# Kernel optimization log

Hardware: AMD Instinct MI355X
Metric: run time of the kernel (lower is better)

## Reference

```python
import jax, jax.numpy as jnp
import numpy as np

N, T, D, H = 64, 512, 1024, 1024

def setup_inputs() -> dict:
    key = jax.random.key(0)
    k1, k2, k3, k4 = jax.random.split(key, 4)
    x = jax.random.normal(k1, (N, T, D), dtype=jnp.float32)
    h0 = jax.random.normal(k2, (N, H), dtype=jnp.float32)
    Wx = jax.random.normal(k3, (D, 4 * H), dtype=jnp.float32) / np.sqrt(D)
    Wh = jax.random.normal(k4, (H, 4 * H), dtype=jnp.float32) / np.sqrt(H)
    b = jnp.zeros((4 * H,), dtype=jnp.float32)
    return {"x": x, "h0": h0, "Wx": Wx, "Wh": Wh, "b": b}

def reference(x, h0, Wx, Wh, b):
    # Hoist the input projection out of the recurrence: (N,T,D)@(D,4H) -> (N,T,4H)
    Hdim = h0.shape[1]
    xW = jnp.einsum('ntd,dg->ntg', x, Wx) + b  # (N, T, 4H)
    c0 = jnp.zeros_like(h0)

    def step(carry, xw_t):
        prev_h, prev_c = carry
        A = xw_t + prev_h @ Wh  # (N, 4H)
        i = jax.nn.sigmoid(A[:, 0:Hdim])
        f = jax.nn.sigmoid(A[:, Hdim:2 * Hdim])
        o = jax.nn.sigmoid(A[:, 2 * Hdim:3 * Hdim])
        g = jnp.tanh(A[:, 3 * Hdim:4 * Hdim])
        next_c = f * prev_c + i * g
        next_h = o * jnp.tanh(next_c)
        return (next_h, next_c), next_h

    # scan over time: xW transposed to (T, N, 4H)
    _, hs = jax.lax.scan(step, (h0, c0), jnp.swapaxes(xW, 0, 1))
    return jnp.swapaxes(hs, 0, 1)  # (N, T, H)
```

## Files before the change

### kernel.cpp

```cpp
#include <hip/hip_runtime.h>
#include <hip/hip_bf16.h>


#define T_T 512
#define KTOT 2048

typedef short bf16x8 __attribute__((ext_vector_type(8)));
typedef float f32x4 __attribute__((ext_vector_type(4)));
typedef unsigned u32x4 __attribute__((ext_vector_type(4)));

union B8U { u32x4 u; bf16x8 v; };
union P4 { __hip_bfloat16 h[4]; uint2 u; };

__device__ __forceinline__ float fsig(float x) {
  float e = __builtin_amdgcn_exp2f(-1.442695041f * x);
  return __builtin_amdgcn_rcpf(1.f + e);
}
__device__ __forceinline__ float ftanh(float x) {
  float e = __builtin_amdgcn_exp2f(2.885390082f * fabsf(x));
  float r = 1.f - 2.f * __builtin_amdgcn_rcpf(e + 1.f);
  return copysignf(r, x);
}

__global__ __launch_bounds__(256) void prep_weights(const float* __restrict__ Wx,
                                                    const float* __restrict__ Wh,
                                                    __hip_bfloat16* __restrict__ Wt) {
  __shared__ float tile[64][65];
  int kb = blockIdx.x & 31;
  int cb = blockIdx.x >> 5;
  int k0 = kb << 6, c0 = cb << 6;
  const float* W = (k0 < 1024) ? Wx : Wh;
  int kr0 = k0 & 1023;
  int tid = threadIdx.x;
  int f4 = tid & 15;
  int i0 = tid >> 4;
  for (int p = 0; p < 4; ++p) {
    int i = i0 + (p << 4);
    float4 v = *(const float4*)(W + (size_t)(kr0 + i) * 4096 + c0 + (f4 << 2));
    tile[(f4 << 2) + 0][i] = v.x;
    tile[(f4 << 2) + 1][i] = v.y;
    tile[(f4 << 2) + 2][i] = v.z;
    tile[(f4 << 2) + 3][i] = v.w;
  }
  __syncthreads();
  for (int p = 0; p < 16; ++p) {
    int idx = (p << 8) + tid;
    int kl = idx & 63, cl = idx >> 6;
    Wt[(size_t)(c0 + cl) * KTOT + k0 + kl] = __float2bfloat16(tile[cl][kl]);
  }
}

__global__ __launch_bounds__(256) void prep_xb(const float* __restrict__ x,
                                               __hip_bfloat16* __restrict__ xb) {
  int b = blockIdx.x;
  int n = b & 63, t = b >> 6;
  const float4* src = (const float4*)(x + ((size_t)n * T_T + t) * 1024);
  __hip_bfloat16* dst = xb + ((size_t)t * 64 + n) * 1024;
  float4 v = src[threadIdx.x];
  P4 pk;
  pk.h[0] = __float2bfloat16(v.x);
  pk.h[1] = __float2bfloat16(v.y);
  pk.h[2] = __float2bfloat16(v.z);
  pk.h[3] = __float2bfloat16(v.w);
  *(uint2*)(dst + (threadIdx.x << 2)) = pk.u;
}

__global__ __launch_bounds__(256) void prep_state(const float* __restrict__ h0,
                                                  __hip_bfloat16* __restrict__ hb) {
  int i = blockIdx.x * 256 + threadIdx.x;
  hb[i] = __float2bfloat16(h0[i]);
}

__global__ __launch_bounds__(512, 2) void lstm_persist(
    const __hip_bfloat16* __restrict__ xb,
    const float* __restrict__ bias,
    const __hip_bfloat16* __restrict__ Wt,
    __hip_bfloat16* hb,
    float* __restrict__ out,
    unsigned* flags)
{
  __shared__ __align__(16) __hip_bfloat16 AX[2][16][1032];
  __shared__ __align__(16) __hip_bfloat16 AH[16][1032];
  __shared__ float gtX[4][16][17];
  __shared__ float gtH[4][16][17];
  __shared__ __align__(16) __hip_bfloat16 hrow[16][16];
  __shared__ unsigned xcnt;

  const int tid  = threadIdx.x;
  const int cgrp = blockIdx.x & 63;
  const int bg   = blockIdx.x >> 6;
  const int rows0 = bg << 4;
  const int lane = tid & 63;
  const int wv   = tid >> 6;
  const int gate = wv & 3;
  const int half = wv >> 2;
  const int mcol = lane & 15;
  const int q    = lane >> 4;
  const int tid2 = tid & 255;

  if (tid == 0) xcnt = 0;

  u32x4 wfrag[32];
  {
    const __hip_bfloat16* wp = Wt
      + ((size_t)(gate << 10) + (cgrp << 4) + mcol) * (size_t)KTOT
      + (half << 10) + (q << 3);
    #pragma unroll
    for (int kk = 0; kk < 32; ++kk)
      wfrag[kk] = *(const u32x4*)(wp + (kk << 5));
  }

  const int er = tid2 >> 4, ej = tid2 & 15;
  const int hcol = (cgrp << 4) + ej;
  const int rg = rows0 + er;
  float b_i = 0.f, b_f = 0.f, b_o = 0.f, b_g = 0.f;
  if (half == 0) {
    b_i = bias[hcol]; b_f = bias[1024 + hcol];
    b_o = bias[2048 + hcol]; b_g = bias[3072 + hcol];
  }
  float creg = 0.f;
  int poison = 0;

  if (half == 0) {
    const u32x4* src = (const u32x4*)(xb + (size_t)rows0 * 1024);
    #pragma unroll
    for (int p = 0; p < 8; ++p) {
      int r = (p << 1) + (tid2 >> 7), c8 = tid2 & 127;
      u32x4 v = src[r * 128 + c8];
      *(u32x4*)&AX[0][r][c8 << 3] = v;
    }
  } else {
    const u32x4* src = (const u32x4*)(hb + (size_t)rows0 * 1024);
    #pragma unroll
    for (int p = 0; p < 8; ++p) {
      int r = (p << 1) + (tid2 >> 7), c8 = tid2 & 127;
      u32x4 v = src[r * 128 + c8];
      *(u32x4*)&AH[r][c8 << 3] = v;
    }
  }
  __syncthreads();

  for (int t = 0; t < T_T; ++t) {
    {
      const __hip_bfloat16* L = (half == 0) ? &AX[t & 1][0][0] : &AH[0][0];
      f32x4 acc = {0.f, 0.f, 0.f, 0.f};
      #pragma unroll
      for (int kk = 0; kk < 32; ++kk) {
        B8U a, b;
        a.u = *(const u32x4*)(L + (size_t)mcol * 1032 + (kk << 5) + (q << 3));
        b.u = wfrag[kk];
        acc = __builtin_amdgcn_mfma_f32_16x16x32_bf16(a.v, b.v, acc, 0, 0, 0);
      }
      float (*gt)[16][17] = (half == 0) ? gtX : gtH;
      #pragma unroll
      for (int i = 0; i < 4; ++i)
        gt[gate][(q << 2) + i][mcol] = acc[i];
    }
    __syncthreads();
    if (half == 0) {
      float av_i = gtX[0][er][ej] + gtH[0][er][ej] + b_i;
      float av_f = gtX[1][er][ej] + gtH[1][er][ej] + b_f;
      float av_o = gtX[2][er][ej] + gtH[2][er][ej] + b_o;
      float av_g = gtX[3][er][ej] + gtH[3][er][ej] + b_g;
      float iv = fsig(av_i), fv = fsig(av_f), ov = fsig(av_o);
      float gv = ftanh(av_g);
      float cn = fv * creg + iv * gv;
      creg = cn;
      float hv = ov * ftanh(cn);
      out[((size_t)rg * T_T + t) * 1024 + hcol] = hv;
      hrow[er][ej] = __float2bfloat16(hv);
      if (lane == 0)
        __hip_atomic_fetch_add(&xcnt, 1u, __ATOMIC_RELAXED, __HIP_MEMORY_SCOPE_WORKGROUP);
      if (wv == 0) {
        int spun = 0;
        while (!poison) {
          unsigned v = __hip_atomic_load(&xcnt, __ATOMIC_RELAXED,
                                         __HIP_MEMORY_SCOPE_WORKGROUP);
          if (v == 4u) break;
          if (++spun > (1 << 20)) poison = 1;
        }
        if (lane < 32) {
          u32x4 v = *(const u32x4*)&hrow[lane >> 1][(lane & 1) << 3];
          __hip_bfloat16* hd = hb + ((size_t)((t + 1) & 1) << 16)
                             + (size_t)(rows0 + (lane >> 1)) * 1024
                             + (cgrp << 4) + ((lane & 1) << 3);
          asm volatile("global_store_dwordx4 %0, %1, off sc0 sc1"
                       :: "v"(hd), "v"(v) : "memory");
        }
        asm volatile("s_waitcnt vmcnt(0)" ::: "memory");
        if (lane == 0) {
          __hip_atomic_store(&xcnt, 0u, __ATOMIC_RELAXED, __HIP_MEMORY_SCOPE_WORKGROUP);
          __hip_atomic_store(flags + ((unsigned)t << 8) + ((unsigned)bg << 6) + cgrp, 1u,
                             __ATOMIC_RELAXED, __HIP_MEMORY_SCOPE_AGENT);
        }
      }
      if (t + 1 < T_T) {
        const u32x4* src = (const u32x4*)(xb + ((size_t)(t + 1) * 64 + rows0) * 1024);
        #pragma unroll
        for (int p = 0; p < 8; ++p) {
          int r = (p << 1) + (tid2 >> 7), c8 = tid2 & 127;
          u32x4 v = src[r * 128 + c8];
          *(u32x4*)&AX[(t + 1) & 1][r][c8 << 3] = v;
        }
      }
    } else if (t + 1 < T_T) {
      const int chunk = wv - 4;
      {
        unsigned* fp = flags + ((unsigned)t << 8) + ((unsigned)bg << 6)
                     + (chunk << 4) + (lane & 15);
        int spun = 0;
        while (!poison) {
          unsigned v = __hip_atomic_load(fp, __ATOMIC_RELAXED, __HIP_MEMORY_SCOPE_AGENT);
          if (__all(v != 0)) break;
          __builtin_amdgcn_s_sleep(1);
          if (++spun > (1 << 16)) poison = 1;
        }
      }
      {
        const __hip_bfloat16* hsrc = hb + ((size_t)((t + 1) & 1) << 16);
        const int c8 = lane & 31;
        const int r0 = lane >> 5;
        const char* base = (const char*)(hsrc + (size_t)(rows0 + r0) * 1024
                                         + (chunk << 8) + (c8 << 3));
        const char* p0 = base;          const char* p1 = base + 4096;
        const char* p2 = base + 8192;   const char* p3 = base + 12288;
        const char* p4 = base + 16384;  const char* p5 = base + 20480;
        const char* p6 = base + 24576;  const char* p7 = base + 28672;
        u32x4 d0, d1, d2, d3, d4, d5, d6, d7;
        asm volatile(
          "global_load_dwordx4 %0, %8, off sc0 sc1\n\t"
          "global_load_dwordx4 %1, %9, off sc0 sc1\n\t"
          "global_load_dwordx4 %2, %10, off sc0 sc1\n\t"
          "global_load_dwordx4 %3, %11, off sc0 sc1\n\t"
          "global_load_dwordx4 %4, %12, off sc0 sc1\n\t"
          "global_load_dwordx4 %5, %13, off sc0 sc1\n\t"
          "global_load_dwordx4 %6, %14, off sc0 sc1\n\t"
          "global_load_dwordx4 %7, %15, off sc0 sc1\n\t"
          "s_waitcnt vmcnt(0)"
          : "=&v"(d0), "=&v"(d1), "=&v"(d2), "=&v"(d3),
            "=&v"(d4), "=&v"(d5), "=&v"(d6), "=&v"(d7)
          : "v"(p0), "v"(p1), "v"(p2), "v"(p3),
            "v"(p4), "v"(p5), "v"(p6), "v"(p7)
          : "memory");
        const int cc = (chunk << 8) + (c8 << 3);
        *(u32x4*)&AH[r0 +  0][cc] = d0;
        *(u32x4*)&AH[r0 +  2][cc] = d1;
        *(u32x4*)&AH[r0 +  4][cc] = d2;
        *(u32x4*)&AH[r0 +  6][cc] = d3;
        *(u32x4*)&AH[r0 +  8][cc] = d4;
        *(u32x4*)&AH[r0 + 10][cc] = d5;
        *(u32x4*)&AH[r0 + 12][cc] = d6;
        *(u32x4*)&AH[r0 + 14][cc] = d7;
      }
    }
    __syncthreads();
  }
}

extern "C" void kernel_launch(void* const* d_in, const int* in_sizes, int n_in,
                              void* d_out, int out_size, void* d_ws, size_t ws_size,
                              hipStream_t stream) {
  const float* x    = (const float*)d_in[0];
  const float* h0   = (const float*)d_in[1];
  const float* Wx   = (const float*)d_in[2];
  const float* Wh   = (const float*)d_in[3];
  const float* bias = (const float*)d_in[4];
  float* out = (float*)d_out;

  char* ws = (char*)d_ws;
  __hip_bfloat16* Wt  = (__hip_bfloat16*)ws;
  __hip_bfloat16* xb  = (__hip_bfloat16*)(ws + ((size_t)16 << 20));
  __hip_bfloat16* hbf = (__hip_bfloat16*)(ws + ((size_t)80 << 20));
  unsigned* flags     = (unsigned*)(ws + ((size_t)80 << 20) + (1u << 18));

  hipLaunchKernelGGL(prep_weights, dim3(2048), dim3(256), 0, stream, Wx, Wh, Wt);
  hipLaunchKernelGGL(prep_xb, dim3(32768), dim3(256), 0, stream, x, xb);
  hipLaunchKernelGGL(prep_state, dim3(256), dim3(256), 0, stream, h0, hbf);
  (void)hipMemsetAsync(flags, 0, (size_t)512 * 4 * 64 * sizeof(unsigned), stream);

  void* kargs[6];
  kargs[0] = (void*)&xb;
  kargs[1] = (void*)&bias;
  kargs[2] = (void*)&Wt;
  kargs[3] = (void*)&hbf;
  kargs[4] = (void*)&out;
  kargs[5] = (void*)&flags;
  (void)hipLaunchCooperativeKernel(lstm_persist, dim3(256), dim3(512), kargs, 0, stream);
}
```

Baseline: 3.792 ms.

## Move x-projection off the critical path and split recurrent matmul across all waves

The x-projection MFMA for step t+1 now runs on the first half of the waves after they publish h_t, using weights streamed from global memory, with double-buffered gate results. The recurrent h@Wh matmul is split in K across all eight waves, halving the serial per-step chain. The change also adds an XOR swizzle to the LDS layout, moves the output store after the flag publication, and removes the sleep from the flag spin. The cost is extra global weight traffic for Wx each step and a shorter spin timeout that could poison earlier.

```diff
diff --git a/kernel.cpp b/kernel.cpp
--- a/kernel.cpp
+++ b/kernel.cpp
@@ -20,6 +20,10 @@
   float e = __builtin_amdgcn_exp2f(2.885390082f * fabsf(x));
   float r = 1.f - 2.f * __builtin_amdgcn_rcpf(e + 1.f);
   return copysignf(r, x);
+}
+
+__device__ __forceinline__ int swz(int r, int cb) {
+  return (r << 11) + (cb ^ ((r & 7) << 4));
 }
 
 __global__ __launch_bounds__(256) void prep_weights(const float* __restrict__ Wx,
@@ -79,10 +83,10 @@
     float* __restrict__ out,
     unsigned* flags)
 {
-  __shared__ __align__(16) __hip_bfloat16 AX[2][16][1032];
-  __shared__ __align__(16) __hip_bfloat16 AH[16][1032];
-  __shared__ float gtX[4][16][17];
-  __shared__ float gtH[4][16][17];
+  __shared__ __align__(16) unsigned char AX[2][32768];
+  __shared__ __align__(16) unsigned char AH[32768];
+  __shared__ float gtH[2][4][16][20];
+  __shared__ float gtX[2][4][16][20];
   __shared__ __align__(16) __hip_bfloat16 hrow[16][16];
   __shared__ unsigned xcnt;
 
@@ -93,6 +97,7 @@
   const int lane = tid & 63;
   const int wv   = tid >> 6;
   const int gate = wv & 3;
+  const int kh   = wv >> 2;
   const int half = wv >> 2;
   const int mcol = lane & 15;
   const int q    = lane >> 4;
@@ -100,15 +105,17 @@
 
   if (tid == 0) xcnt = 0;
 
-  u32x4 wfrag[32];
+  u32x4 wfragH[16];
   {
     const __hip_bfloat16* wp = Wt
       + ((size_t)(gate << 10) + (cgrp << 4) + mcol) * (size_t)KTOT
-      + (half << 10) + (q << 3);
-    #pragma unroll
-    for (int kk = 0; kk < 32; ++kk)
-      wfrag[kk] = *(const u32x4*)(wp + (kk << 5));
-  }
+      + 1024 + (kh << 9) + (q << 3);
+    #pragma unroll
+    for (int kk = 0; kk < 16; ++kk)
+      wfragH[kk] = *(const u32x4*)(wp + (kk << 5));
+  }
+  const __hip_bfloat16* wpx = Wt
+    + ((size_t)(wv << 10) + (cgrp << 4) + mcol) * (size_t)KTOT + (q << 3);
 
   const int er = tid2 >> 4, ej = tid2 & 15;
   const int hcol = (cgrp << 4) + ej;
@@ -127,7 +134,7 @@
     for (int p = 0; p < 8; ++p) {
       int r = (p << 1) + (tid2 >> 7), c8 = tid2 & 127;
       u32x4 v = src[r * 128 + c8];
-      *(u32x4*)&AX[0][r][c8 << 3] = v;
+      *(u32x4*)(&AX[0][0] + swz(r, c8 << 4)) = v;
     }
   } else {
     const u32x4* src = (const u32x4*)(hb + (size_t)rows0 * 1024);
@@ -135,43 +142,64 @@
     for (int p = 0; p < 8; ++p) {
       int r = (p << 1) + (tid2 >> 7), c8 = tid2 & 127;
       u32x4 v = src[r * 128 + c8];
-      *(u32x4*)&AH[r][c8 << 3] = v;
+      *(u32x4*)(&AH[0] + swz(r, c8 << 4)) = v;
+    }
+  }
+  __syncthreads();
+  if (half == 0) {
+    f32x4 a0 = {0,0,0,0}, a1 = {0,0,0,0};
+    #pragma unroll 8
+    for (int kk = 0; kk < 32; ++kk) {
+      B8U a, b;
+      a.u = *(const u32x4*)(&AX[0][0] + swz(mcol, (kk << 6) + (q << 4)));
+      b.u = *(const u32x4*)(wpx + (kk << 5));
+      if (kk & 1) a1 = __builtin_amdgcn_mfma_f32_16x16x32_bf16(a.v, b.v, a1, 0, 0, 0);
+      else        a0 = __builtin_amdgcn_mfma_f32_16x16x32_bf16(a.v, b.v, a0, 0, 0, 0);
+    }
+    #pragma unroll
+    for (int i = 0; i < 4; ++i)
+      gtX[0][gate][(q << 2) + i][mcol] = a0[i] + a1[i];
+    const u32x4* src = (const u32x4*)(xb + ((size_t)64 + rows0) * 1024);
+    #pragma unroll
+    for (int p = 0; p < 8; ++p) {
+      int r = (p << 1) + (tid2 >> 7), c8 = tid2 & 127;
+      u32x4 v = src[r * 128 + c8];
+      *(u32x4*)(&AX[1][0] + swz(r, c8 << 4)) = v;
     }
   }
   __syncthreads();
 
   for (int t = 0; t < T_T; ++t) {
     {
-      const __hip_bfloat16* L = (half == 0) ? &AX[t & 1][0][0] : &AH[0][0];
-      f32x4 acc = {0.f, 0.f, 0.f, 0.f};
+      f32x4 a0 = {0,0,0,0}, a1 = {0,0,0,0};
+      const int kbase = kh << 10;
       #pragma unroll
-      for (int kk = 0; kk < 32; ++kk) {
+      for (int kk = 0; kk < 16; ++kk) {
         B8U a, b;
-        a.u = *(const u32x4*)(L + (size_t)mcol * 1032 + (kk << 5) + (q << 3));
-        b.u = wfrag[kk];
-        acc = __builtin_amdgcn_mfma_f32_16x16x32_bf16(a.v, b.v, acc, 0, 0, 0);
-      }
-      float (*gt)[16][17] = (half == 0) ? gtX : gtH;
+        a.u = *(const u32x4*)(&AH[0] + swz(mcol, kbase + (kk << 6) + (q << 4)));
+        b.u = wfragH[kk];
+        if (kk & 1) a1 = __builtin_amdgcn_mfma_f32_16x16x32_bf16(a.v, b.v, a1, 0, 0, 0);
+        else        a0 = __builtin_amdgcn_mfma_f32_16x16x32_bf16(a.v, b.v, a0, 0, 0, 0);
+      }
       #pragma unroll
       for (int i = 0; i < 4; ++i)
-        gt[gate][(q << 2) + i][mcol] = acc[i];
+        gtH[kh][gate][(q << 2) + i][mcol] = a0[i] + a1[i];
     }
     __syncthreads();
     if (half == 0) {
-      float av_i = gtX[0][er][ej] + gtH[0][er][ej] + b_i;
-      float av_f = gtX[1][er][ej] + gtH[1][er][ej] + b_f;
-      float av_o = gtX[2][er][ej] + gtH[2][er][ej] + b_o;
-      float av_g = gtX[3][er][ej] + gtH[3][er][ej] + b_g;
+      float av_i = gtX[t & 1][0][er][ej] + gtH[0][0][er][ej] + gtH[1][0][er][ej] + b_i;
+      float av_f = gtX[t & 1][1][er][ej] + gtH[0][1][er][ej] + gtH[1][1][er][ej] + b_f;
+      float av_o = gtX[t & 1][2][er][ej] + gtH[0][2][er][ej] + gtH[1][2][er][ej] + b_o;
+      float av_g = gtX[t & 1][3][er][ej] + gtH[0][3][er][ej] + gtH[1][3][er][ej] + b_g;
       float iv = fsig(av_i), fv = fsig(av_f), ov = fsig(av_o);
       float gv = ftanh(av_g);
       float cn = fv * creg + iv * gv;
       creg = cn;
       float hv = ov * ftanh(cn);
-      out[((size_t)rg * T_T + t) * 1024 + hcol] = hv;
       hrow[er][ej] = __float2bfloat16(hv);
       if (lane == 0)
         __hip_atomic_fetch_add(&xcnt, 1u, __ATOMIC_RELAXED, __HIP_MEMORY_SCOPE_WORKGROUP);
-      if (wv == 0) {
+      if (wv == 0 && t + 1 < T_T) {
         int spun = 0;
         while (!poison) {
           unsigned v = __hip_atomic_load(&xcnt, __ATOMIC_RELAXED,
@@ -193,14 +221,33 @@
           __hip_atomic_store(flags + ((unsigned)t << 8) + ((unsigned)bg << 6) + cgrp, 1u,
                              __ATOMIC_RELAXED, __HIP_MEMORY_SCOPE_AGENT);
         }
-      }
+      } else if (wv == 0 && lane == 0) {
+        __hip_atomic_store(&xcnt, 0u, __ATOMIC_RELAXED, __HIP_MEMORY_SCOPE_WORKGROUP);
+      }
+      out[((size_t)rg * T_T + t) * 1024 + hcol] = hv;
       if (t + 1 < T_T) {
-        const u32x4* src = (const u32x4*)(xb + ((size_t)(t + 1) * 64 + rows0) * 1024);
+        const unsigned char* L = &AX[(t + 1) & 1][0];
+        f32x4 a0 = {0,0,0,0}, a1 = {0,0,0,0};
+        #pragma unroll 8
+        for (int kk = 0; kk < 32; ++kk) {
+          B8U a, b;
+          a.u = *(const u32x4*)(L + swz(mcol, (kk << 6) + (q << 4)));
+          b.u = *(const u32x4*)(wpx + (kk << 5));
+          if (kk & 1) a1 = __builtin_amdgcn_mfma_f32_16x16x32_bf16(a.v, b.v, a1, 0, 0, 0);
+          else        a0 = __builtin_amdgcn_mfma_f32_16x16x32_bf16(a.v, b.v, a0, 0, 0, 0);
+        }
+        #pragma unroll
+        for (int i = 0; i < 4; ++i)
+          gtX[(t + 1) & 1][gate][(q << 2) + i][mcol] = a0[i] + a1[i];
+      }
+      if (t + 2 < T_T) {
+        const u32x4* src = (const u32x4*)(xb + ((size_t)(t + 2) * 64 + rows0) * 1024);
+        unsigned char* D = &AX[t & 1][0];
         #pragma unroll
         for (int p = 0; p < 8; ++p) {
           int r = (p << 1) + (tid2 >> 7), c8 = tid2 & 127;
           u32x4 v = src[r * 128 + c8];
-          *(u32x4*)&AX[(t + 1) & 1][r][c8 << 3] = v;
+          *(u32x4*)(D + swz(r, c8 << 4)) = v;
         }
       }
     } else if (t + 1 < T_T) {
@@ -212,8 +259,7 @@
         while (!poison) {
           unsigned v = __hip_atomic_load(fp, __ATOMIC_RELAXED, __HIP_MEMORY_SCOPE_AGENT);
           if (__all(v != 0)) break;
-          __builtin_amdgcn_s_sleep(1);
-          if (++spun > (1 << 16)) poison = 1;
+          if (++spun > (1 << 13)) poison = 1;
         }
       }
       {
@@ -242,15 +288,15 @@
           : "v"(p0), "v"(p1), "v"(p2), "v"(p3),
             "v"(p4), "v"(p5), "v"(p6), "v"(p7)
           : "memory");
-        const int cc = (chunk << 8) + (c8 << 3);
-        *(u32x4*)&AH[r0 +  0][cc] = d0;
-        *(u32x4*)&AH[r0 +  2][cc] = d1;
-        *(u32x4*)&AH[r0 +  4][cc] = d2;
-        *(u32x4*)&AH[r0 +  6][cc] = d3;
-        *(u32x4*)&AH[r0 +  8][cc] = d4;
-        *(u32x4*)&AH[r0 + 10][cc] = d5;
-        *(u32x4*)&AH[r0 + 12][cc] = d6;
-        *(u32x4*)&AH[r0 + 14][cc] = d7;
+        const int cc = (chunk << 9) + (c8 << 4);
+        *(u32x4*)(&AH[0] + swz(r0 +  0, cc)) = d0;
+        *(u32x4*)(&AH[0] + swz(r0 +  2, cc)) = d1;
+        *(u32x4*)(&AH[0] + swz(r0 +  4, cc)) = d2;
+        *(u32x4*)(&AH[0] + swz(r0 +  6, cc)) = d3;
+        *(u32x4*)(&AH[0] + swz(r0 +  8, cc)) = d4;
+        *(u32x4*)(&AH[0] + swz(r0 + 10, cc)) = d5;
+        *(u32x4*)(&AH[0] + swz(r0 + 12, cc)) = d6;
+        *(u32x4*)(&AH[0] + swz(r0 + 14, cc)) = d7;
       }
     }
     __syncthreads();
```

Result: slower. 4.366 ms (+15.2%).

## Prefetch next x tile early, parallelize h publish, lighten barriers in LSTM recurrence

Applied to the files above, without the earlier changes.

Issues the global loads for the next timestep's x tile before the mid-step barrier so their latency overlaps the gate math and handoff. The h row publish is now split across all four gate waves, each storing its own rows, instead of wave 0 storing everything after the counter spin. The output store is moved after the flag signal. __syncthreads is replaced by a barrier that waits only on LDS counters, and an asm pin keeps the weight fragments in registers. The cost is eight more live vector registers per thread, plus reliance on the custom barrier and the store order being correct.

```diff
diff --git a/kernel.cpp b/kernel.cpp
--- a/kernel.cpp
+++ b/kernel.cpp
@@ -21,6 +21,12 @@
   float r = 1.f - 2.f * __builtin_amdgcn_rcpf(e + 1.f);
   return copysignf(r, x);
 }
+
+#define BAR_LGKM() do {                                   \
+    asm volatile("s_waitcnt lgkmcnt(0)" ::: "memory");    \
+    __builtin_amdgcn_s_barrier();                         \
+    __builtin_amdgcn_sched_barrier(0);                    \
+  } while (0)
 
 __global__ __launch_bounds__(256) void prep_weights(const float* __restrict__ Wx,
                                                     const float* __restrict__ Wh,
@@ -108,6 +114,9 @@
     #pragma unroll
     for (int kk = 0; kk < 32; ++kk)
       wfrag[kk] = *(const u32x4*)(wp + (kk << 5));
+    #pragma unroll
+    for (int kk = 0; kk < 32; ++kk)
+      asm volatile("" : "+v"(wfrag[kk]));
   }
 
   const int er = tid2 >> 4, ej = tid2 & 15;
@@ -156,7 +165,16 @@
       for (int i = 0; i < 4; ++i)
         gt[gate][(q << 2) + i][mcol] = acc[i];
     }
-    __syncthreads();
+    u32x4 xld[8];
+    if (half == 0 && t + 1 < T_T) {
+      const u32x4* src = (const u32x4*)(xb + ((size_t)(t + 1) * 64 + rows0) * 1024);
+      #pragma unroll
+      for (int p = 0; p < 8; ++p) {
+        int r = (p << 1) + (tid2 >> 7), c8 = tid2 & 127;
+        xld[p] = src[r * 128 + c8];
+      }
+    }
+    BAR_LGKM();
     if (half == 0) {
       float av_i = gtX[0][er][ej] + gtH[0][er][ej] + b_i;
       float av_f = gtX[1][er][ej] + gtH[1][er][ej] + b_f;
@@ -167,40 +185,43 @@
       float cn = fv * creg + iv * gv;
       creg = cn;
       float hv = ov * ftanh(cn);
-      out[((size_t)rg * T_T + t) * 1024 + hcol] = hv;
       hrow[er][ej] = __float2bfloat16(hv);
-      if (lane == 0)
-        __hip_atomic_fetch_add(&xcnt, 1u, __ATOMIC_RELAXED, __HIP_MEMORY_SCOPE_WORKGROUP);
-      if (wv == 0) {
-        int spun = 0;
-        while (!poison) {
-          unsigned v = __hip_atomic_load(&xcnt, __ATOMIC_RELAXED,
-                                         __HIP_MEMORY_SCOPE_WORKGROUP);
-          if (v == 4u) break;
-          if (++spun > (1 << 20)) poison = 1;
-        }
-        if (lane < 32) {
-          u32x4 v = *(const u32x4*)&hrow[lane >> 1][(lane & 1) << 3];
+      if (t + 1 < T_T) {
+        if (lane < 8) {
+          int row = (wv << 2) + (lane >> 1);
+          u32x4 v = *(const u32x4*)&hrow[row][(lane & 1) << 3];
           __hip_bfloat16* hd = hb + ((size_t)((t + 1) & 1) << 16)
-                             + (size_t)(rows0 + (lane >> 1)) * 1024
+                             + (size_t)(rows0 + row) * 1024
                              + (cgrp << 4) + ((lane & 1) << 3);
           asm volatile("global_store_dwordx4 %0, %1, off sc0 sc1"
                        :: "v"(hd), "v"(v) : "memory");
         }
         asm volatile("s_waitcnt vmcnt(0)" ::: "memory");
-        if (lane == 0) {
-          __hip_atomic_store(&xcnt, 0u, __ATOMIC_RELAXED, __HIP_MEMORY_SCOPE_WORKGROUP);
-          __hip_atomic_store(flags + ((unsigned)t << 8) + ((unsigned)bg << 6) + cgrp, 1u,
-                             __ATOMIC_RELAXED, __HIP_MEMORY_SCOPE_AGENT);
+        if (lane == 0)
+          __hip_atomic_fetch_add(&xcnt, 1u, __ATOMIC_RELAXED,
+                                 __HIP_MEMORY_SCOPE_WORKGROUP);
+        if (wv == 0) {
+          int spun = 0;
+          while (!poison) {
+            unsigned v = __hip_atomic_load(&xcnt, __ATOMIC_RELAXED,
+                                           __HIP_MEMORY_SCOPE_WORKGROUP);
+            if (v == 4u) break;
+            if (++spun > (1 << 20)) poison = 1;
+          }
+          if (lane == 0) {
+            __hip_atomic_store(&xcnt, 0u, __ATOMIC_RELAXED,
+                               __HIP_MEMORY_SCOPE_WORKGROUP);
+            __hip_atomic_store(flags + ((unsigned)t << 8) + ((unsigned)bg << 6) + cgrp,
+                               1u, __ATOMIC_RELAXED, __HIP_MEMORY_SCOPE_AGENT);
+          }
         }
       }
+      out[((size_t)rg * T_T + t) * 1024 + hcol] = hv;
       if (t + 1 < T_T) {
-        const u32x4* src = (const u32x4*)(xb + ((size_t)(t + 1) * 64 + rows0) * 1024);
         #pragma unroll
         for (int p = 0; p < 8; ++p) {
           int r = (p << 1) + (tid2 >> 7), c8 = tid2 & 127;
-          u32x4 v = src[r * 128 + c8];
-          *(u32x4*)&AX[(t + 1) & 1][r][c8 << 3] = v;
+          *(u32x4*)&AX[(t + 1) & 1][r][c8 << 3] = xld[p];
         }
       }
     } else if (t + 1 < T_T) {
@@ -253,7 +274,7 @@
         *(u32x4*)&AH[r0 + 14][cc] = d7;
       }
     }
-    __syncthreads();
+    BAR_LGKM();
   }
 }
 
```

After: 4.264 ms. +12.4%, slower.
